# Kernel tuning notes

Measured on AMD Instinct MI355X. Metric: run time of the kernel, lower is better.

## Reference

```python
import jax, jax.numpy as jnp
import numpy as np

D_MODEL = 1024
NUM_HEADS = 16
D_K = D_MODEL // NUM_HEADS
B, S = 4, 2048


def setup_inputs() -> dict:
    key = jax.random.key(0)
    ks = jax.random.split(key, 12)
    scale = 1.0 / np.sqrt(D_MODEL)
    inp = {
        "Q": jax.random.normal(ks[0], (B, S, D_MODEL), dtype=jnp.float32),
        "K": jax.random.normal(ks[1], (B, S, D_MODEL), dtype=jnp.float32),
        "V": jax.random.normal(ks[2], (B, S, D_MODEL), dtype=jnp.float32),
        # causal mask broadcast over batch and heads; masked_fill where mask==0
        "mask": jnp.tril(jnp.ones((S, S), dtype=jnp.int32))[None, None, :, :],
        "Wq": jax.random.normal(ks[3], (D_MODEL, D_MODEL), dtype=jnp.float32) * scale,
        "bq": jnp.zeros((D_MODEL,), dtype=jnp.float32),
        "Wk": jax.random.normal(ks[4], (D_MODEL, D_MODEL), dtype=jnp.float32) * scale,
        "bk": jnp.zeros((D_MODEL,), dtype=jnp.float32),
        "Wv": jax.random.normal(ks[5], (D_MODEL, D_MODEL), dtype=jnp.float32) * scale,
        "bv": jnp.zeros((D_MODEL,), dtype=jnp.float32),
        "Wo": jax.random.normal(ks[6], (D_MODEL, D_MODEL), dtype=jnp.float32) * scale,
        "bo": jnp.zeros((D_MODEL,), dtype=jnp.float32),
    }
    return inp


def _split_heads(x):
    b, s, _ = x.shape
    return x.reshape(b, s, NUM_HEADS, D_K).transpose(0, 2, 1, 3)  # [B,H,S,Dk]


def reference(Q, K, V, mask, Wq, bq, Wk, bk, Wv, bv, Wo, bo):
    # torch nn.Linear: x @ W.T + b
    q = _split_heads(Q @ Wq.T + bq)
    k = _split_heads(K @ Wk.T + bk)
    v = _split_heads(V @ Wv.T + bv)
    scores = jnp.einsum("bhsd,bhtd->bhst", q, k) / jnp.sqrt(jnp.float32(D_K))
    scores = jnp.where(mask == 0, jnp.float32(-1e9), scores)
    probs = jax.nn.softmax(scores, axis=-1)  # dropout is identity in eval mode
    ctx = jnp.einsum("bhst,bhtd->bhsd", probs, v)
    ctx = ctx.transpose(0, 2, 1, 3).reshape(Q.shape[0], Q.shape[1], D_MODEL)
    out = ctx @ Wo.T + bo
    return out, probs
```

## Files before the change

### kernel.cpp

```cpp
#include <hip/hip_runtime.h>
#include <stdint.h>

typedef unsigned short u16;
typedef unsigned int u32;
typedef __attribute__((ext_vector_type(2))) unsigned int u32x2;
typedef __attribute__((ext_vector_type(8))) short short8;
typedef __attribute__((ext_vector_type(4))) float f32x4;
typedef __attribute__((ext_vector_type(4))) unsigned int u32x4;

#define SEQ 2048
#define DM 1024
#define NH 16
#define NBH 64
#define MR 8192

#define GLOAD16(g, l) __builtin_amdgcn_global_load_lds( \
    (const __attribute__((address_space(1))) void*)(g), \
    (__attribute__((address_space(3))) void*)(l), 16, 0, 0)

#define VMCNT(N) asm volatile("s_waitcnt vmcnt(" #N ")" ::: "memory")

__device__ __forceinline__ u16 f2bf(float f) {
  u32 u = __float_as_uint(f);
  u32 r = u + 0x7fffu + ((u >> 16) & 1u);
  return (u16)(r >> 16);
}
__device__ __forceinline__ u32 cvtpk_bf16(float lo, float hi) {
  u32 r;
  asm("v_cvt_pk_bf16_f32 %0, %1, %2" : "=v"(r) : "v"(lo), "v"(hi));
  return r;
}

__global__ __launch_bounds__(256) void cvt_all(
    const float* __restrict__ Q, const float* __restrict__ K, const float* __restrict__ V,
    const float* __restrict__ Wq, const float* __restrict__ Wk, const float* __restrict__ Wv,
    const float* __restrict__ Wo,
    u16* __restrict__ dQ, u16* __restrict__ dK, u16* __restrict__ dV,
    u16* __restrict__ dWq, u16* __restrict__ dWk, u16* __restrict__ dWv, u16* __restrict__ dWo) {
  int b = blockIdx.x;
  const float* s; u16* d; size_t off;
  if (b < 4096)       { s = Q;  d = dQ;  off = (size_t)b * 2048; }
  else if (b < 8192)  { s = K;  d = dK;  off = (size_t)(b - 4096) * 2048; }
  else if (b < 12288) { s = V;  d = dV;  off = (size_t)(b - 8192) * 2048; }
  else if (b < 12800) { s = Wq; d = dWq; off = (size_t)(b - 12288) * 2048; }
  else if (b < 13312) { s = Wk; d = dWk; off = (size_t)(b - 12800) * 2048; }
  else if (b < 13824) { s = Wv; d = dWv; off = (size_t)(b - 13312) * 2048; }
  else                { s = Wo; d = dWo; off = (size_t)(b - 13824) * 2048; }
  size_t i = off + (size_t)threadIdx.x * 8;
  float4 x = *(const float4*)(s + i);
  float4 y = *(const float4*)(s + i + 4);
  u32x4 o;
  o.x = (u32)f2bf(x.x) | ((u32)f2bf(x.y) << 16);
  o.y = (u32)f2bf(x.z) | ((u32)f2bf(x.w) << 16);
  o.z = (u32)f2bf(y.x) | ((u32)f2bf(y.y) << 16);
  o.w = (u32)f2bf(y.z) | ((u32)f2bf(y.w) << 16);
  *(u32x4*)(d + i) = o;
}

__device__ __forceinline__ void gemm_body(
    const u16* __restrict__ A, const u16* __restrict__ Bw, const float* __restrict__ bias,
    void* __restrict__ Cp, int wg, int MODE) {
  const int bn = wg & 7;
  const int bm = wg >> 3;
  __shared__ u16 As[128 * 64];
  __shared__ u16 Bs[128 * 64];
  const int tid = threadIdx.x;
  const int lane = tid & 63, wave = tid >> 6;
  const int wr = wave >> 1, wc = wave & 1;
  const int g16 = lane >> 4, l16 = lane & 15;
  f32x4 acc[4][4] = {};

  const int srow = lane >> 3;
  const int scol = (lane & 7) * 8;
  const u16* Abase = A + (size_t)(bm * 128) * DM + scol;
  const u16* Bbase = Bw + (size_t)(bn * 128) * DM + scol;

  for (int kt = 0; kt < DM; kt += 64) {
    __syncthreads();
#pragma unroll
    for (int i = 0; i < 4; ++i) {
      const int r0 = wave * 32 + i * 8;
      GLOAD16(Abase + (size_t)(r0 + srow) * DM + kt, (char*)As + r0 * 128);
      GLOAD16(Bbase + (size_t)(r0 + srow) * DM + kt, (char*)Bs + r0 * 128);
    }
    __syncthreads();
#pragma unroll
    for (int ks = 0; ks < 2; ++ks) {
      short8 af[4], bfr[4];
#pragma unroll
      for (int m = 0; m < 4; ++m)
        af[m] = *(const short8*)((const char*)As + (wr * 64 + m * 16 + l16) * 128 + ks * 64 + g16 * 16);
#pragma unroll
      for (int n = 0; n < 4; ++n)
        bfr[n] = *(const short8*)((const char*)Bs + (wc * 64 + n * 16 + l16) * 128 + ks * 64 + g16 * 16);
#pragma unroll
      for (int m = 0; m < 4; ++m)
#pragma unroll
        for (int n = 0; n < 4; ++n)
          acc[m][n] = __builtin_amdgcn_mfma_f32_16x16x32_bf16(af[m], bfr[n], acc[m][n], 0, 0, 0);
    }
  }
#pragma unroll
  for (int m = 0; m < 4; ++m)
#pragma unroll
    for (int n = 0; n < 4; ++n) {
      int col = bn * 128 + wc * 64 + n * 16 + l16;
      float bs = bias[col];
      if (MODE == 2) {
        int row0 = bm * 128 + wr * 64 + m * 16 + g16 * 4;
        int bb = row0 >> 11, ss = row0 & 2047;
        int hh = col >> 6, dd = col & 63;
        u32 lo = (u32)f2bf(acc[m][n][0] + bs) | ((u32)f2bf(acc[m][n][1] + bs) << 16);
        u32 hi = (u32)f2bf(acc[m][n][2] + bs) | ((u32)f2bf(acc[m][n][3] + bs) << 16);
        *(u32x2*)((u16*)Cp + (((size_t)(bb * NH + hh) * 64 + dd) * SEQ + ss)) = (u32x2){lo, hi};
      } else {
#pragma unroll
        for (int r = 0; r < 4; ++r) {
          int row = bm * 128 + wr * 64 + m * 16 + g16 * 4 + r;
          float v = acc[m][n][r] + bs;
          if (MODE == 0) {
            int bb = row >> 11, ss = row & 2047, hh = col >> 6, dd = col & 63;
            ((u16*)Cp)[((((size_t)bb * NH + hh) * SEQ + ss) << 6) + dd] = f2bf(v);
          } else {
            ((float*)Cp)[(size_t)row * DM + col] = v;
          }
        }
      }
    }
}

__global__ __launch_bounds__(256) void gemm_qkv(
    const u16* __restrict__ Qb, const u16* __restrict__ Wqb, const float* __restrict__ bq, u16* __restrict__ qhp,
    const u16* __restrict__ Kb, const u16* __restrict__ Wkb, const float* __restrict__ bk, u16* __restrict__ khp,
    const u16* __restrict__ Vb, const u16* __restrict__ Wvb, const float* __restrict__ bv, u16* __restrict__ vtp) {
  const int bid = blockIdx.x;
  const int sel = bid >> 9;
  const int inner = bid & 511;
  const int wg = (inner & 7) * 64 + (inner >> 3);
  if (sel == 0)      gemm_body(Qb, Wqb, bq, qhp, wg, 0);
  else if (sel == 1) gemm_body(Kb, Wkb, bk, khp, wg, 0);
  else               gemm_body(Vb, Wvb, bv, vtp, wg, 2);
}

__global__ __launch_bounds__(256) void gemm_out(
    const u16* __restrict__ A, const u16* __restrict__ Bw, const float* __restrict__ bias,
    float* __restrict__ Cp) {
  const int bid = blockIdx.x;
  const int wg = (bid & 7) * 64 + (bid >> 3);
  gemm_body(A, Bw, bias, Cp, wg, 1);
}

__global__ __launch_bounds__(512, 4) void attn_fwd(
    const u16* __restrict__ qh, const u16* __restrict__ kh, const u16* __restrict__ vt,
    float* __restrict__ probs, u16* __restrict__ ctx) {
  const int bid = blockIdx.x;
  const int wg = (bid & 7) * 128 + (bid >> 3);
  const int qt = 15 - (wg & 15);
  const int bh = wg >> 4;
  const int tid = threadIdx.x;
  const int lane = tid & 63, wave = tid >> 6;
  const int g16 = lane >> 4, l16 = lane & 15;
  __shared__ __align__(16) char SLDS[65536];
  char* Ps = SLDS + 49152;

  const int qglob = qt * 128 + wave * 16 + l16;
  short8 qf0, qf1;
  {
    const u16* qp = qh + ((size_t)bh * SEQ + qglob) * 64 + g16 * 8;
    qf0 = *(const short8*)qp;
    qf1 = *(const short8*)(qp + 32);
  }
  float lrow = 0.f;
  const float SL2 = 0.125f * 1.44269504088896f;

  const int srow = wave * 8 + (lane >> 3);
  const int sblk = (lane & 7) ^ (lane >> 3);
  const u16* kS = kh + ((size_t)bh * SEQ + srow) * 64 + sblk * 8;
  const u16* vS = vt + ((size_t)bh * 64 + srow) * SEQ + sblk * 8;

  auto qk64 = [&](const char* Kb, int ss, f32x4 (&sc)[4]) {
#pragma unroll
    for (int ks = 0; ks < 2; ++ks) {
      const short8 qf = ks ? qf1 : qf0;
#pragma unroll
      for (int f = 0; f < 4; ++f) {
        const int t = ss * 64 + f * 16 + l16;
        const short8 kb = *(const short8*)(Kb + ((t * 128 + ks * 64 + g16 * 16) ^ ((t & 7) << 4)));
        sc[f] = __builtin_amdgcn_mfma_f32_16x16x32_bf16(kb, qf, sc[f], 0, 0, 0);
      }
    }
  };

  const int nkA = qt + 1;
  auto stageA = [&](int kt) {
#pragma unroll
    for (int i = 0; i < 2; ++i)
      GLOAD16(kS + ((size_t)kt * 128 + i * 64) * 64,
              SLDS + (kt & 3) * 16384 + i * 8192 + wave * 1024);
  };
  stageA(0);
  if (nkA > 1) stageA(1);
  for (int kt = 0; kt < nkA; ++kt) {
    if (kt + 2 < nkA) { stageA(kt + 2); VMCNT(4); }
    else if (kt + 1 < nkA) VMCNT(2);
    else VMCNT(0);
    __builtin_amdgcn_s_barrier();
    const char* Kb = SLDS + (kt & 3) * 16384;
    float s = 0.f;
#pragma unroll
    for (int ss = 0; ss < 2; ++ss) {
      f32x4 sc[4] = {};
      __builtin_amdgcn_s_setprio(1);
      qk64(Kb, ss, sc);
      __builtin_amdgcn_s_setprio(0);
#pragma unroll
      for (int f = 0; f < 4; ++f)
#pragma unroll
        for (int r = 0; r < 4; ++r) {
          const int k = kt * 128 + ss * 64 + f * 16 + g16 * 4 + r;
          s += (k <= qglob) ? exp2f(sc[f][r] * SL2) : 0.f;
        }
    }
    s += __shfl_xor(s, 16);
    s += __shfl_xor(s, 32);
    lrow += s;
  }
  const float rinv = 1.f / lrow;

  f32x4 acc[4] = {};
  const size_t prowB = ((size_t)bh * SEQ + qglob) * SEQ;
  const int prow = wave * 16 + l16;
  const int nkt = 2 * qt + 2;

  __syncthreads();
  auto stageBK = [&](int kt) {
    GLOAD16(kS + (size_t)kt * 4096, SLDS + (kt % 3) * 8192 + wave * 1024);
  };
  auto stageBV = [&](int kt) {
    GLOAD16(vS + (size_t)kt * 64, SLDS + 24576 + (kt % 3) * 8192 + wave * 1024);
  };
  stageBK(0); stageBV(0);
  for (int kt = 0; kt < nkt; ++kt) {
    if (kt + 1 < nkt) {
      stageBK(kt + 1); stageBV(kt + 1);
      if (kt == 0) VMCNT(2); else VMCNT(6);
    } else {
      if (kt == 0) VMCNT(0); else VMCNT(4);
    }
    __builtin_amdgcn_s_barrier();
    const char* Kb = SLDS + (kt % 3) * 8192;
    const char* Vb = SLDS + 24576 + (kt % 3) * 8192;
    f32x4 sc[4] = {};
    __builtin_amdgcn_s_setprio(1);
    qk64(Kb, 0, sc);
    __builtin_amdgcn_s_setprio(0);
#pragma unroll
    for (int f = 0; f < 4; ++f) {
      float pv[4];
#pragma unroll
      for (int r = 0; r < 4; ++r) {
        const int k = kt * 64 + f * 16 + g16 * 4 + r;
        pv[r] = (k <= qglob) ? exp2f(sc[f][r] * SL2) * rinv : 0.f;
      }
      *(f32x4*)(probs + prowB + kt * 64 + f * 16 + g16 * 4) =
          (f32x4){pv[0], pv[1], pv[2], pv[3]};
      u32x2 pk = {cvtpk_bf16(pv[0], pv[1]), cvtpk_bf16(pv[2], pv[3])};
      *(u32x2*)(Ps + ((prow * 128 + f * 32 + g16 * 8) ^ ((prow & 7) << 4))) = pk;
    }
    __builtin_amdgcn_s_setprio(1);
#pragma unroll
    for (int ks = 0; ks < 2; ++ks) {
      const short8 pa = *(const short8*)(Ps + ((prow * 128 + ks * 64 + g16 * 16) ^ ((prow & 7) << 4)));
#pragma unroll
      for (int cf = 0; cf < 4; ++cf) {
        const int dd = cf * 16 + l16;
        const short8 vb = *(const short8*)(Vb + ((dd * 128 + ks * 64 + g16 * 16) ^ ((dd & 7) << 4)));
        acc[cf] = __builtin_amdgcn_mfma_f32_16x16x32_bf16(pa, vb, acc[cf], 0, 0, 0);
      }
    }
    __builtin_amdgcn_s_setprio(0);
  }

  {
    const size_t zrow = ((size_t)bh * SEQ + qt * 128 + wave * 16 + (lane >> 2)) * SEQ;
    const int pcol = (lane & 3) * 16;
    const f32x4 z = {0.f, 0.f, 0.f, 0.f};
    for (int c0 = nkt * 64 + pcol; c0 < SEQ; c0 += 64) {
      float* dst = probs + zrow + c0;
      *(f32x4*)(dst) = z;
      *(f32x4*)(dst + 4) = z;
      *(f32x4*)(dst + 8) = z;
      *(f32x4*)(dst + 12) = z;
    }
  }

#pragma unroll
  for (int cf = 0; cf < 4; ++cf)
#pragma unroll
    for (int r = 0; r < 4; ++r) {
      const int srw = qt * 128 + wave * 16 + g16 * 4 + r;
      const size_t o = ((size_t)(bh >> 4) * SEQ + srw) * DM + (bh & 15) * 64 + cf * 16 + l16;
      ctx[o] = f2bf(acc[cf][r]);
    }
}

extern "C" void kernel_launch(void* const* d_in, const int* in_sizes, int n_in,
                              void* d_out, int out_size, void* d_ws, size_t ws_size,
                              hipStream_t stream) {
  (void)in_sizes; (void)n_in; (void)out_size; (void)ws_size;
  const float* Q  = (const float*)d_in[0];
  const float* K  = (const float*)d_in[1];
  const float* V  = (const float*)d_in[2];
  const float* Wq = (const float*)d_in[4];
  const float* bq = (const float*)d_in[5];
  const float* Wk = (const float*)d_in[6];
  const float* bk = (const float*)d_in[7];
  const float* Wv = (const float*)d_in[8];
  const float* bv = (const float*)d_in[9];
  const float* Wo = (const float*)d_in[10];
  const float* bo = (const float*)d_in[11];

  char* ws = (char*)d_ws;
  const size_t MB = 1024 * 1024;
  u16* Qb  = (u16*)(ws + 0 * MB);
  u16* Kb  = (u16*)(ws + 16 * MB);
  u16* Vb  = (u16*)(ws + 32 * MB);
  u16* Wqb = (u16*)(ws + 48 * MB);
  u16* Wkb = (u16*)(ws + 50 * MB);
  u16* Wvb = (u16*)(ws + 52 * MB);
  u16* Wob = (u16*)(ws + 54 * MB);
  u16* qhp = (u16*)(ws + 56 * MB);
  u16* khp = (u16*)(ws + 72 * MB);
  u16* vtp = (u16*)(ws + 88 * MB);
  u16* ctx = Kb;

  float* outp = (float*)d_out;
  float* probs = outp + (size_t)MR * DM;

  cvt_all<<<14336, 256, 0, stream>>>(Q, K, V, Wq, Wk, Wv, Wo, Qb, Kb, Vb, Wqb, Wkb, Wvb, Wob);
  gemm_qkv<<<1536, 256, 0, stream>>>(Qb, Wqb, bq, qhp, Kb, Wkb, bk, khp, Vb, Wvb, bv, vtp);
  attn_fwd<<<1024, 512, 0, stream>>>(qhp, khp, vtp, probs, ctx);
  gemm_out<<<512, 256, 0, stream>>>(ctx, Wob, bo, outp);
}
```

Baseline: 497.5 us.

## Double-buffer GEMM LDS tiles with XOR swizzle and skip mask checks on full tiles

The projection GEMM now keeps two LDS buffers per operand, so the global-to-LDS load of the next k-tile is issued while the current one is being computed, and each k-tile needs one barrier instead of two. Global source columns and LDS reads use an XOR swizzle on the row index to reduce LDS bank conflicts. In both attention passes, tiles that lie entirely below the causal diagonal skip the per-element mask comparison. The cost is double the GEMM LDS footprint, which may lower occupancy.

Result: faster. 472.0 us (-5.1%).

```diff
diff --git a/kernel.cpp b/kernel.cpp
--- a/kernel.cpp
+++ b/kernel.cpp
@@ -62,8 +62,8 @@
     void* __restrict__ Cp, int wg, int MODE) {
   const int bn = wg & 7;
   const int bm = wg >> 3;
-  __shared__ u16 As[128 * 64];
-  __shared__ u16 Bs[128 * 64];
+  __shared__ u16 As[2][128 * 64];
+  __shared__ u16 Bs[2][128 * 64];
   const int tid = threadIdx.x;
   const int lane = tid & 63, wave = tid >> 6;
   const int wr = wave >> 1, wc = wave & 1;
@@ -71,28 +71,39 @@
   f32x4 acc[4][4] = {};
 
   const int srow = lane >> 3;
-  const int scol = (lane & 7) * 8;
-  const u16* Abase = A + (size_t)(bm * 128) * DM + scol;
-  const u16* Bbase = Bw + (size_t)(bn * 128) * DM + scol;
-
-  for (int kt = 0; kt < DM; kt += 64) {
-    __syncthreads();
+  const int sblk = (lane & 7) ^ srow;
+  const u16* Abase = A + (size_t)(bm * 128) * DM + sblk * 8;
+  const u16* Bbase = Bw + (size_t)(bn * 128) * DM + sblk * 8;
+
+  auto stage = [&](int kt) {
 #pragma unroll
     for (int i = 0; i < 4; ++i) {
       const int r0 = wave * 32 + i * 8;
-      GLOAD16(Abase + (size_t)(r0 + srow) * DM + kt, (char*)As + r0 * 128);
-      GLOAD16(Bbase + (size_t)(r0 + srow) * DM + kt, (char*)Bs + r0 * 128);
-    }
-    __syncthreads();
+      GLOAD16(Abase + (size_t)(r0 + srow) * DM + kt * 64, (char*)As[kt & 1] + r0 * 128);
+      GLOAD16(Bbase + (size_t)(r0 + srow) * DM + kt * 64, (char*)Bs[kt & 1] + r0 * 128);
+    }
+  };
+
+  stage(0);
+  for (int kt = 0; kt < 16; ++kt) {
+    VMCNT(0);
+    __builtin_amdgcn_s_barrier();
+    if (kt + 1 < 16) stage(kt + 1);
+    const char* Ab = (const char*)As[kt & 1];
+    const char* Bb = (const char*)Bs[kt & 1];
 #pragma unroll
     for (int ks = 0; ks < 2; ++ks) {
       short8 af[4], bfr[4];
 #pragma unroll
-      for (int m = 0; m < 4; ++m)
-        af[m] = *(const short8*)((const char*)As + (wr * 64 + m * 16 + l16) * 128 + ks * 64 + g16 * 16);
-#pragma unroll
-      for (int n = 0; n < 4; ++n)
-        bfr[n] = *(const short8*)((const char*)Bs + (wc * 64 + n * 16 + l16) * 128 + ks * 64 + g16 * 16);
+      for (int m = 0; m < 4; ++m) {
+        const int r = wr * 64 + m * 16 + l16;
+        af[m] = *(const short8*)(Ab + ((r * 128 + ks * 64 + g16 * 16) ^ ((r & 7) << 4)));
+      }
+#pragma unroll
+      for (int n = 0; n < 4; ++n) {
+        const int r = wc * 64 + n * 16 + l16;
+        bfr[n] = *(const short8*)(Bb + ((r * 128 + ks * 64 + g16 * 16) ^ ((r & 7) << 4)));
+      }
 #pragma unroll
       for (int m = 0; m < 4; ++m)
 #pragma unroll
@@ -213,13 +224,22 @@
       __builtin_amdgcn_s_setprio(1);
       qk64(Kb, ss, sc);
       __builtin_amdgcn_s_setprio(0);
-#pragma unroll
-      for (int f = 0; f < 4; ++f)
-#pragma unroll
-        for (int r = 0; r < 4; ++r) {
-          const int k = kt * 128 + ss * 64 + f * 16 + g16 * 4 + r;
-          s += (k <= qglob) ? exp2f(sc[f][r] * SL2) : 0.f;
-        }
+      const bool fullt = (kt * 128 + ss * 64 + 63 <= qt * 128 + wave * 16);
+      if (fullt) {
+#pragma unroll
+        for (int f = 0; f < 4; ++f)
+#pragma unroll
+          for (int r = 0; r < 4; ++r)
+            s += exp2f(sc[f][r] * SL2);
+      } else {
+#pragma unroll
+        for (int f = 0; f < 4; ++f)
+#pragma unroll
+          for (int r = 0; r < 4; ++r) {
+            const int k = kt * 128 + ss * 64 + f * 16 + g16 * 4 + r;
+            s += (k <= qglob) ? exp2f(sc[f][r] * SL2) : 0.f;
+          }
+      }
     }
     s += __shfl_xor(s, 16);
     s += __shfl_xor(s, 32);
@@ -254,13 +274,19 @@
     __builtin_amdgcn_s_setprio(1);
     qk64(Kb, 0, sc);
     __builtin_amdgcn_s_setprio(0);
+    const bool fullt = (kt * 64 + 63 <= qt * 128 + wave * 16);
 #pragma unroll
     for (int f = 0; f < 4; ++f) {
       float pv[4];
-#pragma unroll
-      for (int r = 0; r < 4; ++r) {
-        const int k = kt * 64 + f * 16 + g16 * 4 + r;
-        pv[r] = (k <= qglob) ? exp2f(sc[f][r] * SL2) * rinv : 0.f;
+      if (fullt) {
+#pragma unroll
+        for (int r = 0; r < 4; ++r) pv[r] = exp2f(sc[f][r] * SL2) * rinv;
+      } else {
+#pragma unroll
+        for (int r = 0; r < 4; ++r) {
+          const int k = kt * 64 + f * 16 + g16 * 4 + r;
+          pv[r] = (k <= qglob) ? exp2f(sc[f][r] * SL2) * rinv : 0.f;
+        }
       }
       *(f32x4*)(probs + prowB + kt * 64 + f * 16 + g16 * 4) =
           (f32x4){pv[0], pv[1], pv[2], pv[3]};
```
